# Kernel optimization log

Measured on AMD Instinct MI355X. Metric: run time of the kernel, lower is better.

The kernel has to match this reference:

```python
import jax, jax.numpy as jnp
import numpy as np

L = 65536   # path length
D = 6       # path channels
K = 4       # signature truncation depth (max of sig_orders)


def setup_inputs() -> dict:
    key = jax.random.key(0)
    # scale keeps high-order signature terms numerically tame over 65k steps
    x = jax.random.normal(key, (L, D), dtype=jnp.float32) * 0.05
    return {"x": x}


def _signature(x):
    """Truncated path signature (levels 1..K), flattened, via Chen's relation.

    Signature of one linear segment with increment dx is exp(dx) in the
    tensor algebra: level k term = dx^{(x)k} / k!.  Full-path signature is the
    Chen (tensor-algebra) product of the per-segment exponentials, computed
    with a left-fold scan over increments.
    """
    dx = x[1:] - x[:-1]                       # (N, D) increments
    N = dx.shape[0]
    # Vectorized exp(dx) levels: E[k-1] = dx^{(x)k}/k!, flattened (N, D^k)
    E = [dx]
    for k in range(2, K + 1):
        Ek = jnp.einsum('na,nb->nab', E[-1], dx).reshape(N, -1) / k
        E.append(Ek)

    S0 = tuple(jnp.zeros((D ** (k + 1),), dtype=x.dtype) for k in range(K))

    def chen(S, e):
        # T_k = S_k + e_k + sum_{i=1}^{k-1} S_i (x) e_{k-i}   (S_0 = e_0 = 1)
        T = []
        for k in range(K):
            t = S[k] + e[k]
            for i in range(k):
                t = t + jnp.einsum('a,b->ab', S[i], e[k - 1 - i]).reshape(-1)
            T.append(t)
        return tuple(T), None

    S, _ = jax.lax.scan(chen, S0, tuple(E))
    # flatten levels 1..K: shape (D + D^2 + ... + D^K,) = (1554,)
    return jnp.concatenate(S)


def reference(x):
    return _signature(x)
```

## Files before the change

### kernel.cpp

```cpp
#include <hip/hip_runtime.h>

#define DIM 6
#define NSEG 65535
#define CH 64
#define NCHUNK 1024

#define PSTRIDE 1568
#define PL1 0
#define PL2 8
#define PL3 48
#define PL4 264
#define NGRP 259

__global__ __launch_bounds__(64) void sig_fold(const float* __restrict__ x,
                                               float* __restrict__ part) {
    __shared__ float dxs[CH * 8];
    const int t = threadIdx.x;
    const int c = blockIdx.x;
    const int j0 = c * CH;
    const int cnt = min(CH, NSEG - j0);

    for (int f = t; f < CH * 8; f += 64) dxs[f] = 0.f;
    __syncthreads();
    const float* xb = x + (size_t)j0 * DIM;
    for (int f = t; f < cnt * DIM; f += 64) {
        int j = f / 6, k = f - j * 6;
        dxs[j * 8 + k] = xb[f + 6] - xb[f];
    }
    __syncthreads();

    const int ab = (t < 36) ? t : 35;
    const int a = ab / 6, b = ab - a * 6;
    const float* dxap = dxs + a;
    const float* dxbp = dxs + b;

    float r4[36], r3[6], r2 = 0.f, s1 = 0.f;
#pragma unroll
    for (int i = 0; i < 36; ++i) r4[i] = 0.f;
#pragma unroll
    for (int i = 0; i < 6; ++i) r3[i] = 0.f;

#pragma unroll 2
    for (int j = 0; j < CH; ++j) {
        const float4 q0 = *(const float4*)(dxs + j * 8);
        const float2 q1 = *(const float2*)(dxs + j * 8 + 4);
        const float dxv[6] = {q0.x, q0.y, q0.z, q0.w, q1.x, q1.y};
        const float dxa = dxap[j * 8];
        const float dxb = dxbp[j * 8];

        float t2 = fmaf(dxb, fmaf(dxa, (1.f / 12.f), s1 * (1.f / 3.f)), r2);
        float t2h = 0.5f * t2;
        float w[6];
#pragma unroll
        for (int cc = 0; cc < 6; ++cc) w[cc] = fmaf(t2h, dxv[cc], r3[cc]);
#pragma unroll
        for (int cc = 0; cc < 6; ++cc)
#pragma unroll
            for (int d = 0; d < 6; ++d)
                r4[cc * 6 + d] = fmaf(w[cc], dxv[d], r4[cc * 6 + d]);
        float t3 = fmaf(dxa, (1.f / 3.f), s1);
        float v = fmaf(0.5f * t3, dxb, r2);
#pragma unroll
        for (int cc = 0; cc < 6; ++cc) r3[cc] = fmaf(v, dxv[cc], r3[cc]);
        r2 = fmaf(fmaf(0.5f, dxa, s1), dxb, r2);
        s1 += dxa;
    }

    if (t < 36) {
        float* P = part + (size_t)c * PSTRIDE;
        if (a == b) P[PL1 + a] = s1;
        P[PL2 + ab] = r2;
        float* p3 = P + PL3 + ab * 6;
        *(float2*)(p3 + 0) = make_float2(r3[0], r3[1]);
        *(float2*)(p3 + 2) = make_float2(r3[2], r3[3]);
        *(float2*)(p3 + 4) = make_float2(r3[4], r3[5]);
        float* p4 = P + PL4 + ab * 36;
#pragma unroll
        for (int i = 0; i < 9; ++i)
            *(float4*)(p4 + 4 * i) =
                make_float4(r4[4 * i], r4[4 * i + 1], r4[4 * i + 2], r4[4 * i + 3]);
    }
}

__device__ __forceinline__ void chen_vals(const float* __restrict__ A,
                                          const float* __restrict__ B,
                                          int g, float* v) {
    if (g == 0) {
#pragma unroll
        for (int d = 0; d < 6; ++d) v[d] = A[PL1 + d] + B[PL1 + d];
    } else if (g < 7) {
        int a = g - 1;
        float a1 = A[PL1 + a];
        const float* Ar = A + PL2 + a * 6;
        const float* Br = B + PL2 + a * 6;
#pragma unroll
        for (int d = 0; d < 6; ++d) v[d] = Ar[d] + Br[d] + a1 * B[PL1 + d];
    } else if (g < 43) {
        int ab = g - 7, a = ab / 6, b = ab - a * 6;
        float a2 = A[PL2 + ab], a1 = A[PL1 + a];
        const float* Ar = A + PL3 + ab * 6;
        const float* Br = B + PL3 + ab * 6;
        const float* B2r = B + PL2 + b * 6;
#pragma unroll
        for (int d = 0; d < 6; ++d)
            v[d] = Ar[d] + Br[d] + a2 * B[PL1 + d] + a1 * B2r[d];
    } else {
        int abc = g - 43, ab = abc / 6, cc = abc - ab * 6, a = abc / 36,
            bc = abc - a * 36;
        float a3 = A[PL3 + abc], a2 = A[PL2 + ab], a1 = A[PL1 + a];
        const float* Ar = A + PL4 + abc * 6;
        const float* Br = B + PL4 + abc * 6;
        const float* B2r = B + PL2 + cc * 6;
        const float* B3r = B + PL3 + bc * 6;
#pragma unroll
        for (int d = 0; d < 6; ++d)
            v[d] = Ar[d] + Br[d] + a3 * B[PL1 + d] + a2 * B2r[d] + a1 * B3r[d];
    }
}

__device__ __forceinline__ int grp_off_padded(int g) {
    if (g == 0) return PL1;
    if (g < 7) return PL2 + (g - 1) * 6;
    if (g < 43) return PL3 + (g - 7) * 6;
    return PL4 + (g - 43) * 6;
}
__device__ __forceinline__ int grp_off_flat(int g) {
    if (g == 0) return 0;
    if (g < 7) return 6 + (g - 1) * 6;
    if (g < 43) return 42 + (g - 7) * 6;
    return 258 + (g - 43) * 6;
}

__device__ __forceinline__ void write_final(float* out, int flat_out, int g,
                                            const float* v, int blk) {
    if (flat_out) {
        int off = grp_off_flat(g);
#pragma unroll
        for (int d = 0; d < 6; ++d) out[off + d] = v[d];
    } else {
        float* O = out + (size_t)blk * PSTRIDE;
        int off = grp_off_padded(g);
#pragma unroll
        for (int d = 0; d < 6; ++d) O[off + d] = v[d];
    }
}

__global__ __launch_bounds__(256) void sig_tree(const float* __restrict__ in,
                                                float* __restrict__ out,
                                                int gs, int flat_out) {
    __shared__ float buf0[4 * PSTRIDE];
    __shared__ float buf1[2 * PSTRIDE];
    const int t = threadIdx.x;
    const float* gbase = in + (size_t)blockIdx.x * gs * PSTRIDE;

    int np = gs >> 1;
    for (int idx = t; idx < np * NGRP; idx += 256) {
        int p = idx / NGRP, g = idx - p * NGRP;
        const float* A = gbase + (size_t)(2 * p) * PSTRIDE;
        float v[6];
        chen_vals(A, A + PSTRIDE, g, v);
        if (np == 1) {
            write_final(out, flat_out, g, v, blockIdx.x);
        } else {
            float* o = buf0 + p * PSTRIDE + grp_off_padded(g);
#pragma unroll
            for (int d = 0; d < 6; ++d) o[d] = v[d];
        }
    }
    if (np == 1) return;

    float* cur = buf0;
    float* nxt = buf1;
    while (np > 1) {
        __syncthreads();
        np >>= 1;
        for (int idx = t; idx < np * NGRP; idx += 256) {
            int p = idx / NGRP, g = idx - p * NGRP;
            const float* A = cur + (2 * p) * PSTRIDE;
            float v[6];
            chen_vals(A, A + PSTRIDE, g, v);
            if (np == 1) {
                write_final(out, flat_out, g, v, blockIdx.x);
            } else {
                float* o = nxt + p * PSTRIDE + grp_off_padded(g);
#pragma unroll
                for (int d = 0; d < 6; ++d) o[d] = v[d];
            }
        }
        float* tmp = cur; cur = nxt; nxt = tmp;
    }
}

extern "C" void kernel_launch(void* const* d_in, const int* in_sizes, int n_in,
                              void* d_out, int out_size, void* d_ws, size_t ws_size,
                              hipStream_t stream) {
    const float* x = (const float*)d_in[0];
    float* out = (float*)d_out;
    float* ws0 = (float*)d_ws;
    float* ws1 = ws0 + (size_t)NCHUNK * PSTRIDE;
    float* ws2 = ws1 + (size_t)128 * PSTRIDE;
    float* ws3 = ws2 + (size_t)16 * PSTRIDE;

    sig_fold<<<NCHUNK, 64, 0, stream>>>(x, ws0);
    sig_tree<<<128, 256, 0, stream>>>(ws0, ws1, 8, 0);
    sig_tree<<<16, 256, 0, stream>>>(ws1, ws2, 8, 0);
    sig_tree<<<2, 256, 0, stream>>>(ws2, ws3, 8, 0);
    sig_tree<<<1, 256, 0, stream>>>(ws3, out, 2, 1);
}
```

Measured before the change: 101.0 us.

## Fuse first tree levels into 4-wave fold blocks and cut kernel launches

Measured after the change: 136.6 us. 35.2% more time.

```diff
diff --git a/kernel.cpp b/kernel.cpp
--- a/kernel.cpp
+++ b/kernel.cpp
@@ -2,8 +2,10 @@
 
 #define DIM 6
 #define NSEG 65535
-#define CH 64
-#define NCHUNK 1024
+#define CH 16
+#define WPB 4
+#define NCHUNK 4096
+#define NBLK (NCHUNK / WPB)
 
 #define PSTRIDE 1568
 #define PL1 0
@@ -11,76 +13,6 @@
 #define PL3 48
 #define PL4 264
 #define NGRP 259
-
-__global__ __launch_bounds__(64) void sig_fold(const float* __restrict__ x,
-                                               float* __restrict__ part) {
-    __shared__ float dxs[CH * 8];
-    const int t = threadIdx.x;
-    const int c = blockIdx.x;
-    const int j0 = c * CH;
-    const int cnt = min(CH, NSEG - j0);
-
-    for (int f = t; f < CH * 8; f += 64) dxs[f] = 0.f;
-    __syncthreads();
-    const float* xb = x + (size_t)j0 * DIM;
-    for (int f = t; f < cnt * DIM; f += 64) {
-        int j = f / 6, k = f - j * 6;
-        dxs[j * 8 + k] = xb[f + 6] - xb[f];
-    }
-    __syncthreads();
-
-    const int ab = (t < 36) ? t : 35;
-    const int a = ab / 6, b = ab - a * 6;
-    const float* dxap = dxs + a;
-    const float* dxbp = dxs + b;
-
-    float r4[36], r3[6], r2 = 0.f, s1 = 0.f;
-#pragma unroll
-    for (int i = 0; i < 36; ++i) r4[i] = 0.f;
-#pragma unroll
-    for (int i = 0; i < 6; ++i) r3[i] = 0.f;
-
-#pragma unroll 2
-    for (int j = 0; j < CH; ++j) {
-        const float4 q0 = *(const float4*)(dxs + j * 8);
-        const float2 q1 = *(const float2*)(dxs + j * 8 + 4);
-        const float dxv[6] = {q0.x, q0.y, q0.z, q0.w, q1.x, q1.y};
-        const float dxa = dxap[j * 8];
-        const float dxb = dxbp[j * 8];
-
-        float t2 = fmaf(dxb, fmaf(dxa, (1.f / 12.f), s1 * (1.f / 3.f)), r2);
-        float t2h = 0.5f * t2;
-        float w[6];
-#pragma unroll
-        for (int cc = 0; cc < 6; ++cc) w[cc] = fmaf(t2h, dxv[cc], r3[cc]);
-#pragma unroll
-        for (int cc = 0; cc < 6; ++cc)
-#pragma unroll
-            for (int d = 0; d < 6; ++d)
-                r4[cc * 6 + d] = fmaf(w[cc], dxv[d], r4[cc * 6 + d]);
-        float t3 = fmaf(dxa, (1.f / 3.f), s1);
-        float v = fmaf(0.5f * t3, dxb, r2);
-#pragma unroll
-        for (int cc = 0; cc < 6; ++cc) r3[cc] = fmaf(v, dxv[cc], r3[cc]);
-        r2 = fmaf(fmaf(0.5f, dxa, s1), dxb, r2);
-        s1 += dxa;
-    }
-
-    if (t < 36) {
-        float* P = part + (size_t)c * PSTRIDE;
-        if (a == b) P[PL1 + a] = s1;
-        P[PL2 + ab] = r2;
-        float* p3 = P + PL3 + ab * 6;
-        *(float2*)(p3 + 0) = make_float2(r3[0], r3[1]);
-        *(float2*)(p3 + 2) = make_float2(r3[2], r3[3]);
-        *(float2*)(p3 + 4) = make_float2(r3[4], r3[5]);
-        float* p4 = P + PL4 + ab * 36;
-#pragma unroll
-        for (int i = 0; i < 9; ++i)
-            *(float4*)(p4 + 4 * i) =
-                make_float4(r4[4 * i], r4[4 * i + 1], r4[4 * i + 2], r4[4 * i + 3]);
-    }
-}
 
 __device__ __forceinline__ void chen_vals(const float* __restrict__ A,
                                           const float* __restrict__ B,
@@ -145,11 +77,105 @@
     }
 }
 
+__global__ __launch_bounds__(256) void sig_fold4(const float* __restrict__ x,
+                                                 float* __restrict__ part) {
+    __shared__ float dxs[WPB * CH * 8];
+    __shared__ float P[WPB * PSTRIDE];
+    __shared__ float Q[2 * PSTRIDE];
+    const int t = threadIdx.x;
+    const int w = t >> 6;
+    const int lane = t & 63;
+    const int c = blockIdx.x * WPB + w;
+    const int j0 = c * CH;
+    const int cnt = min(CH, NSEG - j0);
+
+    float* dxw = dxs + w * (CH * 8);
+    for (int f = lane; f < CH * 8; f += 64) dxw[f] = 0.f;
+    __syncthreads();
+    const float* xb = x + (size_t)j0 * DIM;
+    for (int f = lane; f < cnt * DIM; f += 64) {
+        int j = f / 6, k = f - j * 6;
+        dxw[j * 8 + k] = xb[f + 6] - xb[f];
+    }
+    __syncthreads();
+
+    const int ab = (lane < 36) ? lane : 35;
+    const int a = ab / 6, b = ab - a * 6;
+    const float* dxap = dxw + a;
+    const float* dxbp = dxw + b;
+
+    float r4[36], r3[6], r2 = 0.f, s1 = 0.f;
+#pragma unroll
+    for (int i = 0; i < 36; ++i) r4[i] = 0.f;
+#pragma unroll
+    for (int i = 0; i < 6; ++i) r3[i] = 0.f;
+
+#pragma unroll 2
+    for (int j = 0; j < CH; ++j) {
+        const float4 q0 = *(const float4*)(dxw + j * 8);
+        const float2 q1 = *(const float2*)(dxw + j * 8 + 4);
+        const float dxv[6] = {q0.x, q0.y, q0.z, q0.w, q1.x, q1.y};
+        const float dxa = dxap[j * 8];
+        const float dxb = dxbp[j * 8];
+
+        float t2 = fmaf(dxb, fmaf(dxa, (1.f / 12.f), s1 * (1.f / 3.f)), r2);
+        float t2h = 0.5f * t2;
+        float wv[6];
+#pragma unroll
+        for (int cc = 0; cc < 6; ++cc) wv[cc] = fmaf(t2h, dxv[cc], r3[cc]);
+#pragma unroll
+        for (int cc = 0; cc < 6; ++cc)
+#pragma unroll
+            for (int d = 0; d < 6; ++d)
+                r4[cc * 6 + d] = fmaf(wv[cc], dxv[d], r4[cc * 6 + d]);
+        float t3 = fmaf(dxa, (1.f / 3.f), s1);
+        float v = fmaf(0.5f * t3, dxb, r2);
+#pragma unroll
+        for (int cc = 0; cc < 6; ++cc) r3[cc] = fmaf(v, dxv[cc], r3[cc]);
+        r2 = fmaf(fmaf(0.5f, dxa, s1), dxb, r2);
+        s1 += dxa;
+    }
+
+    if (lane < 36) {
+        float* Pw = P + w * PSTRIDE;
+        if (a == b) Pw[PL1 + a] = s1;
+        Pw[PL2 + ab] = r2;
+        float* p3 = Pw + PL3 + ab * 6;
+        *(float2*)(p3 + 0) = make_float2(r3[0], r3[1]);
+        *(float2*)(p3 + 2) = make_float2(r3[2], r3[3]);
+        *(float2*)(p3 + 4) = make_float2(r3[4], r3[5]);
+        float* p4 = Pw + PL4 + ab * 36;
+#pragma unroll
+        for (int i = 0; i < 9; ++i)
+            *(float4*)(p4 + 4 * i) =
+                make_float4(r4[4 * i], r4[4 * i + 1], r4[4 * i + 2], r4[4 * i + 3]);
+    }
+    __syncthreads();
+
+    for (int idx = t; idx < 2 * NGRP; idx += 256) {
+        int p = idx / NGRP, g = idx - p * NGRP;
+        float v[6];
+        chen_vals(P + (2 * p) * PSTRIDE, P + (2 * p + 1) * PSTRIDE, g, v);
+        float* o = Q + p * PSTRIDE + grp_off_padded(g);
+#pragma unroll
+        for (int d = 0; d < 6; ++d) o[d] = v[d];
+    }
+    __syncthreads();
+
+    for (int idx = t; idx < NGRP; idx += 256) {
+        float v[6];
+        chen_vals(Q, Q + PSTRIDE, idx, v);
+        float* O = part + (size_t)blockIdx.x * PSTRIDE + grp_off_padded(idx);
+#pragma unroll
+        for (int d = 0; d < 6; ++d) O[d] = v[d];
+    }
+}
+
 __global__ __launch_bounds__(256) void sig_tree(const float* __restrict__ in,
                                                 float* __restrict__ out,
                                                 int gs, int flat_out) {
-    __shared__ float buf0[4 * PSTRIDE];
-    __shared__ float buf1[2 * PSTRIDE];
+    __shared__ float buf0[16 * PSTRIDE];
+    __shared__ float buf1[8 * PSTRIDE];
     const int t = threadIdx.x;
     const float* gbase = in + (size_t)blockIdx.x * gs * PSTRIDE;
 
@@ -197,13 +223,9 @@
     const float* x = (const float*)d_in[0];
     float* out = (float*)d_out;
     float* ws0 = (float*)d_ws;
-    float* ws1 = ws0 + (size_t)NCHUNK * PSTRIDE;
-    float* ws2 = ws1 + (size_t)128 * PSTRIDE;
-    float* ws3 = ws2 + (size_t)16 * PSTRIDE;
-
-    sig_fold<<<NCHUNK, 64, 0, stream>>>(x, ws0);
-    sig_tree<<<128, 256, 0, stream>>>(ws0, ws1, 8, 0);
-    sig_tree<<<16, 256, 0, stream>>>(ws1, ws2, 8, 0);
-    sig_tree<<<2, 256, 0, stream>>>(ws2, ws3, 8, 0);
-    sig_tree<<<1, 256, 0, stream>>>(ws3, out, 2, 1);
-}
+    float* ws1 = ws0 + (size_t)NBLK * PSTRIDE;
+
+    sig_fold4<<<NBLK, 256, 0, stream>>>(x, ws0);
+    sig_tree<<<32, 256, 0, stream>>>(ws0, ws1, 32, 0);
+    sig_tree<<<1, 256, 0, stream>>>(ws1, out, 32, 1);
+}
```
